# Optimization experiments

Hardware: AMD Instinct MI355X
Metric: run time of the kernel (lower is better)

The kernel has to match this reference:

```python
import jax, jax.numpy as jnp
import numpy as np
import math

MAX_FREQ = 3
OMEGA = 0.5 * math.pi
C = (2 * MAX_FREQ + 1) ** 2  # 49
SQRT2 = math.sqrt(2.0)


def setup_inputs() -> dict:
    key = jax.random.key(0)
    N = 2_000_000
    x = jax.random.normal(key, (N, 3 * C + 2), dtype=jnp.float32)
    return {"x": x}


def _embed(v):
    # v: [N] scalar coordinate -> [N, 2*max_freq+1]
    # order matches torch: [1, sqrt2*cos(1w), sqrt2*sin(1w), cos(2w), sin(2w), ...]
    t = v * OMEGA
    freqs = jnp.arange(1, MAX_FREQ + 1, dtype=t.dtype)  # [F]
    tf = t[:, None] * freqs  # [N, F]
    cs = jnp.stack([SQRT2 * jnp.cos(tf), SQRT2 * jnp.sin(tf)], axis=-1)  # [N, F, 2]
    inter = cs.reshape(v.shape[0], -1)  # [N, 2F] interleaved cos/sin
    ones = jnp.ones((v.shape[0], 1), dtype=t.dtype)
    return jnp.concatenate([ones, inter], axis=-1)  # [N, 2F+1]


def reference(x):
    x = x.reshape(-1, x.shape[-1])  # [N, 3c+2]
    rel = x[:, -2:]
    latent = x[:, :-2]  # [N, 3c]
    N = x.shape[0]
    X = _embed(rel[:, 0])  # [N, 7]
    Y = _embed(rel[:, 1])  # [N, 7]
    # outer product X^T Y flattened row-major over (x_dim, y_dim) -> [N, 49]
    ope_flat = (X[:, :, None] * Y[:, None, :]).reshape(N, -1)
    lat = latent.reshape(N, 3, C)  # channels R,G,B contiguous in torch layout
    out = jnp.einsum('nc,nkc->nk', ope_flat, lat)  # [N, 3]
    return out / 100.0
```

## Files before the change

### kernel.cpp

```cpp
#include <hip/hip_runtime.h>
#include <stdint.h>
#include <math.h>


#define RL      149
#define RTILE   32
#define TILE_B  (RTILE * RL * 4)
#define FULLCH  18
#define OVOFF   (TILE_B - 1024)
#define NLOAD   19
#define GRID    1024
#define NK      3

typedef const __attribute__((address_space(1))) unsigned int as1_uint;
typedef __attribute__((address_space(3))) unsigned int as3_uint;

__device__ __forceinline__ void stage_tile(const char* __restrict__ src,
                                           char* dst, int lane) {
    #pragma unroll
    for (int ci = 0; ci < FULLCH; ++ci)
        __builtin_amdgcn_global_load_lds((as1_uint*)(src + ci * 1024 + lane * 16),
                                         (as3_uint*)(dst + ci * 1024), 16, 0, 0);
    __builtin_amdgcn_global_load_lds((as1_uint*)(src + OVOFF + lane * 16),
                                     (as3_uint*)(dst + OVOFF), 16, 0, 0);
}

__device__ __forceinline__ void compute_row(const float* __restrict__ row,
                                            float* __restrict__ dst) {
    const float OMEGA = 1.5707963267948966f;
    const float S2    = 1.4142135623730951f;
    const float t0 = row[147] * OMEGA;
    const float t1 = row[148] * OMEGA;
    float X[7], Y[7];
    X[0] = 1.f; Y[0] = 1.f;
    #pragma unroll
    for (int f = 1; f <= 3; ++f) {
        float s, c;
        __sincosf(t0 * (float)f, &s, &c);
        X[2*f-1] = S2 * c; X[2*f] = S2 * s;
        __sincosf(t1 * (float)f, &s, &c);
        Y[2*f-1] = S2 * c; Y[2*f] = S2 * s;
    }
    float a0 = 0.f, a1 = 0.f, a2 = 0.f;
    #pragma unroll
    for (int i = 0; i < 7; ++i)
        #pragma unroll
        for (int j = 0; j < 7; ++j) {
            const float p = X[i] * Y[j];
            const int c = i * 7 + j;
            a0 = fmaf(p, row[c],      a0);
            a1 = fmaf(p, row[49 + c], a1);
            a2 = fmaf(p, row[98 + c], a2);
        }
    dst[0] = a0 * 0.01f; dst[1] = a1 * 0.01f; dst[2] = a2 * 0.01f;
}

__global__ __launch_bounds__(64)
void ope_kernel(const float* __restrict__ x, float* __restrict__ out, int nrows) {
    __shared__ __align__(16) char lds[2 * TILE_B];
    const int lane = threadIdx.x;
    const char* __restrict__ xb = (const char*)x;
    const int ntile = nrows / RTILE;
    const long long tfirst = blockIdx.x;
    const int GW = gridDim.x;

    if (tfirst < ntile) stage_tile(xb + tfirst * TILE_B, lds, lane);

    int p = 0;
    for (long long t = tfirst; t < ntile; t += GW, p ^= 1) {
        const long long tn = t + GW;
        if (tn < ntile) {
            stage_tile(xb + tn * TILE_B, lds + (p ^ 1) * TILE_B, lane);
            asm volatile("s_waitcnt vmcnt(19)" ::: "memory");
        } else {
            asm volatile("s_waitcnt vmcnt(0)" ::: "memory");
        }
        __builtin_amdgcn_sched_barrier(0);

        if (lane < RTILE) {
            const float* row = (const float*)(lds + p * TILE_B) + lane * RL;
            float o[NK];
            compute_row(row, o);
            float* __restrict__ dst = out + (t * RTILE + lane) * NK;
            dst[0] = o[0]; dst[1] = o[1]; dst[2] = o[2];
        }
    }

    if (blockIdx.x == 0) {
        for (int r = ntile * RTILE + lane; r < nrows; r += 64) {
            const float* row = x + (long long)r * RL;
            float o[NK];
            compute_row(row, o);
            float* dst = out + (long long)r * NK;
            dst[0] = o[0]; dst[1] = o[1]; dst[2] = o[2];
        }
    }
}

extern "C" void kernel_launch(void* const* d_in, const int* in_sizes, int n_in,
                              void* d_out, int out_size, void* d_ws, size_t ws_size,
                              hipStream_t stream) {
    const float* x = (const float*)d_in[0];
    float* out = (float*)d_out;
    const int nrows = in_sizes[0] / RL;
    ope_kernel<<<GRID, 64, 0, stream>>>(x, out, nrows);
}
```

Before: 219.5 us.

## Replace persistent double-buffered tile loop with one-tile-per-block launch

Drops the persistent grid of 1024 blocks that double-buffered tiles in LDS. The kernel now launches one 64-thread block per 32-row tile, staging that tile into a single LDS buffer and waiting for it before computing. This halves LDS per block so more blocks fit per CU, and latency is hidden by having many resident blocks instead of in-block prefetch. The trade-off is about 62.5k block launches and the loss of explicit load/compute overlap inside each block.

```diff
diff --git a/kernel.cpp b/kernel.cpp
--- a/kernel.cpp
+++ b/kernel.cpp
@@ -8,22 +8,10 @@
 #define TILE_B  (RTILE * RL * 4)
 #define FULLCH  18
 #define OVOFF   (TILE_B - 1024)
-#define NLOAD   19
-#define GRID    1024
 #define NK      3
 
 typedef const __attribute__((address_space(1))) unsigned int as1_uint;
 typedef __attribute__((address_space(3))) unsigned int as3_uint;
-
-__device__ __forceinline__ void stage_tile(const char* __restrict__ src,
-                                           char* dst, int lane) {
-    #pragma unroll
-    for (int ci = 0; ci < FULLCH; ++ci)
-        __builtin_amdgcn_global_load_lds((as1_uint*)(src + ci * 1024 + lane * 16),
-                                         (as3_uint*)(dst + ci * 1024), 16, 0, 0);
-    __builtin_amdgcn_global_load_lds((as1_uint*)(src + OVOFF + lane * 16),
-                                     (as3_uint*)(dst + OVOFF), 16, 0, 0);
-}
 
 __device__ __forceinline__ void compute_row(const float* __restrict__ row,
                                             float* __restrict__ dst) {
@@ -57,37 +45,31 @@
 
 __global__ __launch_bounds__(64)
 void ope_kernel(const float* __restrict__ x, float* __restrict__ out, int nrows) {
-    __shared__ __align__(16) char lds[2 * TILE_B];
+    __shared__ __align__(16) char lds[TILE_B];
     const int lane = threadIdx.x;
-    const char* __restrict__ xb = (const char*)x;
-    const int ntile = nrows / RTILE;
-    const long long tfirst = blockIdx.x;
-    const int GW = gridDim.x;
+    const long long row0 = (long long)blockIdx.x * RTILE;
+    const int vr_full = (row0 + RTILE <= nrows);
 
-    if (tfirst < ntile) stage_tile(xb + tfirst * TILE_B, lds, lane);
-
-    int p = 0;
-    for (long long t = tfirst; t < ntile; t += GW, p ^= 1) {
-        const long long tn = t + GW;
-        if (tn < ntile) {
-            stage_tile(xb + tn * TILE_B, lds + (p ^ 1) * TILE_B, lane);
-            asm volatile("s_waitcnt vmcnt(19)" ::: "memory");
-        } else {
-            asm volatile("s_waitcnt vmcnt(0)" ::: "memory");
-        }
+    if (vr_full) {
+        const char* __restrict__ src = (const char*)x + row0 * RL * 4;
+        #pragma unroll
+        for (int ci = 0; ci < FULLCH; ++ci)
+            __builtin_amdgcn_global_load_lds((as1_uint*)(src + ci * 1024 + lane * 16),
+                                             (as3_uint*)(lds + ci * 1024), 16, 0, 0);
+        __builtin_amdgcn_global_load_lds((as1_uint*)(src + OVOFF + lane * 16),
+                                         (as3_uint*)(lds + OVOFF), 16, 0, 0);
+        asm volatile("s_waitcnt vmcnt(0)" ::: "memory");
         __builtin_amdgcn_sched_barrier(0);
 
         if (lane < RTILE) {
-            const float* row = (const float*)(lds + p * TILE_B) + lane * RL;
+            const float* row = (const float*)lds + lane * RL;
             float o[NK];
             compute_row(row, o);
-            float* __restrict__ dst = out + (t * RTILE + lane) * NK;
+            float* __restrict__ dst = out + (row0 + lane) * NK;
             dst[0] = o[0]; dst[1] = o[1]; dst[2] = o[2];
         }
-    }
-
-    if (blockIdx.x == 0) {
-        for (int r = ntile * RTILE + lane; r < nrows; r += 64) {
+    } else {
+        for (int r = (int)row0 + lane; r < nrows; r += 64) {
             const float* row = x + (long long)r * RL;
             float o[NK];
             compute_row(row, o);
@@ -103,5 +85,6 @@
     const float* x = (const float*)d_in[0];
     float* out = (float*)d_out;
     const int nrows = in_sizes[0] / RL;
-    ope_kernel<<<GRID, 64, 0, stream>>>(x, out, nrows);
+    const int grid = (nrows + RTILE - 1) / RTILE;
+    ope_kernel<<<grid, 64, 0, stream>>>(x, out, nrows);
 }
```

New measurement: 213.2 us. 2.8% less time.
